# Kernel optimization log

Hardware: AMD Instinct MI355X
Metric: run time of the kernel (lower is better)

Reference implementation:

```python
import jax, jax.numpy as jnp
import numpy as np

D = 1024
H = 16
HD = D // H

def setup_inputs() -> dict:
    key = jax.random.key(0)
    ks = jax.random.split(key, 6)
    tokens = jax.random.normal(ks[0], (2, 2048, D), dtype=jnp.float32)
    # LayerNorm params
    ln_gamma = jnp.ones((D,), dtype=jnp.float32)
    ln_beta = jnp.zeros((D,), dtype=jnp.float32)
    # qkv Linear (no bias): torch Linear weight is [3D, D]; store as [D, 3D] for x @ W
    w_qkv = jax.random.normal(ks[1], (D, 3 * D), dtype=jnp.float32) / np.sqrt(D)
    # output projection with bias
    w_proj = jax.random.normal(ks[2], (D, D), dtype=jnp.float32) / np.sqrt(D)
    b_proj = jax.random.normal(ks[3], (D,), dtype=jnp.float32) * 0.01
    return {"tokens": tokens, "ln_gamma": ln_gamma, "ln_beta": ln_beta,
            "w_qkv": w_qkv, "w_proj": w_proj, "b_proj": b_proj}

def reference(tokens, ln_gamma, ln_beta, w_qkv, w_proj, b_proj):
    B, S, _ = tokens.shape
    res = tokens
    # LayerNorm (eps=1e-5, torch default)
    mu = jnp.mean(tokens, axis=-1, keepdims=True)
    var = jnp.var(tokens, axis=-1, keepdims=True)
    x = (tokens - mu) * jax.lax.rsqrt(var + 1e-5) * ln_gamma + ln_beta
    # QKV projection -> [B, S, 3, H, HD] -> q,k,v each [B, H, S, HD]
    qkv = (x @ w_qkv).reshape(B, S, 3, H, HD)
    qkv = jnp.transpose(qkv, (2, 0, 3, 1, 4))
    q, k, v = qkv[0], qkv[1], qkv[2]
    scale = HD ** -0.5
    scores = jnp.einsum('bhsd,bhtd->bhst', q, k) * scale  # [B,H,S,S]
    attn = jax.nn.softmax(scores, axis=-1)
    dots = jnp.einsum('bhst,bhtd->bhsd', attn, v)          # [B,H,S,HD]
    dots = jnp.transpose(dots, (0, 2, 1, 3)).reshape(B, S, D)
    out = dots @ w_proj + b_proj
    return out + res
```

## Files before the change

### kernel.cpp

```cpp
#include <hip/hip_runtime.h>

typedef __bf16 bf16x8 __attribute__((ext_vector_type(8)));
typedef __bf16 bf16x4 __attribute__((ext_vector_type(4)));
typedef float f32x4 __attribute__((ext_vector_type(4)));
typedef unsigned short us8 __attribute__((ext_vector_type(8)));

__device__ __forceinline__ unsigned short f2bf(float f) {
  unsigned int u = __builtin_bit_cast(unsigned int, f);
  u += 0x7FFFu + ((u >> 16) & 1u);
  return (unsigned short)(u >> 16);
}
__device__ __forceinline__ float bf2f(unsigned short s) {
  return __builtin_bit_cast(float, (unsigned int)s << 16);
}

__device__ __forceinline__ void load_lds16(const void* g, void* l) {
  __builtin_amdgcn_global_load_lds(
      (const __attribute__((address_space(1))) unsigned int*)g,
      (__attribute__((address_space(3))) unsigned int*)l, 16, 0, 0);
}

#define MFMA16(a, b, c) __builtin_amdgcn_mfma_f32_16x16x32_bf16(a, b, c, 0, 0, 0)
#define EXP2(x) __builtin_amdgcn_exp2f(x)

constexpr int Dm = 1024, Ss = 2048;

__global__ __launch_bounds__(256) void prep_kernel(
    const float* __restrict__ x, const float* __restrict__ gamma,
    const float* __restrict__ beta, unsigned short* __restrict__ xbf,
    const float* __restrict__ wqkv, unsigned short* __restrict__ wqkvT,
    const float* __restrict__ wproj, unsigned short* __restrict__ wprojT) {
  __shared__ float tile[32][33];
  const int t = threadIdx.x;
  if (blockIdx.x < 4096) {
    const int row = blockIdx.x;
    const float4 v = reinterpret_cast<const float4*>(x + (size_t)row * Dm)[t];
    float s = v.x + v.y + v.z + v.w;
    float ss = v.x * v.x + v.y * v.y + v.z * v.z + v.w * v.w;
#pragma unroll
    for (int off = 1; off < 64; off <<= 1) {
      s += __shfl_xor(s, off);
      ss += __shfl_xor(ss, off);
    }
    float* sb = &tile[0][0];
    const int lane = t & 63, wid = t >> 6;
    if (lane == 0) { sb[wid] = s; sb[4 + wid] = ss; }
    __syncthreads();
    s = sb[0] + sb[1] + sb[2] + sb[3];
    ss = sb[4] + sb[5] + sb[6] + sb[7];
    const float mu = s * (1.0f / Dm);
    const float var = ss * (1.0f / Dm) - mu * mu;
    const float rs = rsqrtf(var + 1e-5f);
    const float4 g = reinterpret_cast<const float4*>(gamma)[t];
    const float4 bt = reinterpret_cast<const float4*>(beta)[t];
    ushort4 pack;
    pack.x = f2bf((v.x - mu) * rs * g.x + bt.x);
    pack.y = f2bf((v.y - mu) * rs * g.y + bt.y);
    pack.z = f2bf((v.z - mu) * rs * g.z + bt.z);
    pack.w = f2bf((v.w - mu) * rs * g.w + bt.w);
    reinterpret_cast<ushort4*>(xbf + (size_t)row * Dm)[t] = pack;
  } else {
    const float* in;
    unsigned short* out;
    int N, bxi, byi;
    const int id0 = blockIdx.x - 4096;
    if (id0 < 3072) {
      in = wqkv; out = wqkvT; N = 3072;
      bxi = id0 % 96; byi = id0 / 96;
    } else {
      in = wproj; out = wprojT; N = 1024;
      const int id = id0 - 3072;
      bxi = id % 32; byi = id / 32;
    }
    const int tx = t & 31, ty = t >> 5;
    const int n0 = bxi * 32, k0 = byi * 32;
#pragma unroll
    for (int i = 0; i < 4; i++)
      tile[ty + i * 8][tx] = in[(size_t)(k0 + ty + i * 8) * N + n0 + tx];
    __syncthreads();
#pragma unroll
    for (int i = 0; i < 4; i++)
      out[(size_t)(n0 + ty + i * 8) * 1024 + k0 + tx] = f2bf(tile[tx][ty + i * 8]);
  }
}

__global__ __launch_bounds__(512) void gemm256_kernel(
    const unsigned short* __restrict__ A, const unsigned short* __restrict__ Bt,
    unsigned short* __restrict__ Cbf, unsigned short* __restrict__ vt) {
  extern __shared__ char lds[];
  const int tid = threadIdx.x;
  const int lane = tid & 63, wid = tid >> 6;
  const int l15 = lane & 15, lg = lane >> 4;
  const int wr = wid >> 2, wc = wid & 3;
  const int lb = (blockIdx.x & 7) * 24 + (blockIdx.x >> 3);
  const int bx = lb % 12, by = lb / 12;
  const int bm = by * 256, bn = bx * 256;
  const int sswz = ((lane & 3) * 16) ^ (((lane >> 3) & 3) << 4);
  const char* Asrc = (const char*)A + (size_t)(bm + wid * 32 + (lane >> 2)) * 2048 + sswz;
  const char* Bsrc = (const char*)Bt + (size_t)(bn + wid * 32 + (lane >> 2)) * 2048 + sswz;
  const int rdsz = ((lg * 16) ^ (((l15 >> 1) & 3) << 4));

#define STG_A(kk_, bufT, tile_)                                                 \
  if ((tile_) < 16) {                                                           \
    _Pragma("unroll") for (int c = 0; c < 2; c++)                               \
      load_lds16(Asrc + (size_t)(c * 16) * 2048 + (tile_) * 128 + (kk_) * 64,   \
                 lds + ((bufT) * 2 + (kk_)) * 16384 + wid * 2048 + c * 1024);   \
  }
#define STG_B(kk_, bufT, tile_)                                                 \
  if ((tile_) < 16) {                                                           \
    _Pragma("unroll") for (int c = 0; c < 2; c++)                               \
      load_lds16(Bsrc + (size_t)(c * 16) * 2048 + (tile_) * 128 + (kk_) * 64,   \
                 lds + 65536 + ((bufT) * 2 + (kk_)) * 16384 + wid * 2048 +      \
                     c * 1024);                                                 \
  }
#define DS_A(buf_, kk_)                                                         \
  _Pragma("unroll") for (int mi = 0; mi < 8; mi++) {                            \
    const int r = wr * 128 + mi * 16 + l15;                                     \
    af[mi] = *(const bf16x8*)(lds + ((buf_) * 2 + (kk_)) * 16384 + r * 64 + rdsz); \
  }
#define DS_B(buf_, kk_, nh_)                                                    \
  _Pragma("unroll") for (int nj = 0; nj < 2; nj++) {                            \
    const int r = wc * 64 + (nh_) * 32 + nj * 16 + l15;                         \
    bfr[nj] = *(const bf16x8*)(lds + 65536 + ((buf_) * 2 + (kk_)) * 16384 +     \
                               r * 64 + rdsz);                                  \
  }
#define MM(nh_)                                                                 \
  __builtin_amdgcn_s_setprio(1);                                                \
  _Pragma("unroll") for (int mi = 0; mi < 8; mi++)                              \
      _Pragma("unroll") for (int nj = 0; nj < 2; nj++)                          \
          acc[mi][(nh_) * 2 + nj] = MFMA16(af[mi], bfr[nj], acc[mi][(nh_) * 2 + nj]); \
  __builtin_amdgcn_s_setprio(0);
#define GBAR __builtin_amdgcn_s_barrier()
#define LGKM0 asm volatile("s_waitcnt lgkmcnt(0)" ::: "memory")

  f32x4 acc[8][4] = {};

  STG_A(0, 0, 0); STG_B(0, 0, 0); STG_A(1, 0, 0); STG_B(1, 0, 0);
  STG_A(0, 1, 1); STG_B(0, 1, 1); STG_A(1, 1, 1);
  asm volatile("s_waitcnt vmcnt(6)" ::: "memory");
  GBAR;

  for (int i = 0; i < 8; ++i) {
    const int t2 = 2 * i + 2, t3 = 2 * i + 3;
    const bool last = (i == 7);
    bf16x8 af[8], bfr[2];
    DS_A(0, 0); DS_B(0, 0, 0); STG_B(1, 1, 2 * i + 1);
    GBAR; LGKM0; MM(0); GBAR;
    DS_B(0, 0, 1); STG_A(0, 0, t2);
    GBAR; LGKM0; MM(1); GBAR;
    DS_A(0, 1); DS_B(0, 1, 0); STG_B(0, 0, t2);
    GBAR; LGKM0; MM(0); GBAR;
    DS_B(0, 1, 1); STG_A(1, 0, t2);
    GBAR; LGKM0; MM(1);
    if (last) asm volatile("s_waitcnt vmcnt(0)" ::: "memory");
    else      asm volatile("s_waitcnt vmcnt(6)" ::: "memory");
    GBAR;
    DS_A(1, 0); DS_B(1, 0, 0); STG_B(1, 0, t2);
    GBAR; LGKM0; MM(0); GBAR;
    DS_B(1, 0, 1); STG_A(0, 1, t3);
    GBAR; LGKM0; MM(1); GBAR;
    DS_A(1, 1); DS_B(1, 1, 0); STG_B(0, 1, t3);
    GBAR; LGKM0; MM(0); GBAR;
    DS_B(1, 1, 1); STG_A(1, 1, t3);
    GBAR; LGKM0; MM(1);
    if (last) asm volatile("s_waitcnt vmcnt(0)" ::: "memory");
    else      asm volatile("s_waitcnt vmcnt(6)" ::: "memory");
    GBAR;
  }

#pragma unroll
  for (int mi = 0; mi < 8; mi++)
#pragma unroll
    for (int nj = 0; nj < 4; nj++) {
      const int m = bm + wr * 128 + mi * 16 + lg * 4;
      const int n = bn + wc * 64 + nj * 16 + l15;
      if (n < 2048) {
        const float sc = (n < 1024) ? 0.180336880f : 1.0f;
#pragma unroll
        for (int r = 0; r < 4; r++)
          Cbf[(size_t)(m + r) * 3072 + n] = f2bf(acc[mi][nj][r] * sc);
      } else {
        const int h = (n - 2048) >> 6, hd = (n - 2048) & 63;
        const int bq = m >> 11, s = m & 2047;
        bf16x4 o;
#pragma unroll
        for (int r = 0; r < 4; r++) o[r] = (__bf16)acc[mi][nj][r];
        *(bf16x4*)(vt + ((size_t)((bq << 4) + h) * 64 + hd) * 2048 + s) = o;
      }
    }
#undef STG_A
#undef STG_B
#undef DS_A
#undef DS_B
#undef MM
#undef GBAR
#undef LGKM0
}

__global__ __launch_bounds__(256) void gemm_proj_kernel(
    const unsigned short* __restrict__ A, const unsigned short* __restrict__ Bt,
    float* __restrict__ Cf, const float* __restrict__ bias,
    const float* __restrict__ resid) {
  __shared__ unsigned short Al[2][128 * 64];
  __shared__ unsigned short Bl[2][64 * 64];
  const int tid = threadIdx.x;
  const int lane = tid & 63, wid = tid >> 6;
  const int l15 = lane & 15, lg = lane >> 4;
  const int wm = wid >> 1, wn = wid & 1;
  const int cpx = gridDim.x >> 3;
  const int lb = (blockIdx.x & 7) * cpx + (blockIdx.x >> 3);
  const int bx = lb % 16, by = lb / 16;
  const int bm = by * 128, bn = bx * 64;
  const int r8 = lane >> 3;
  const int swz = ((lane & 7) * 16) ^ (r8 << 4);
  const char* Ab = (const char*)A;
  const char* Bb = (const char*)Bt;
  f32x4 acc[4][2] = {};

#define PSTAGE(bufi, k0v)                                                      \
  {                                                                            \
    _Pragma("unroll") for (int p = 0; p < 4; p++) {                            \
      const int row = p * 32 + wid * 8 + r8;                                   \
      load_lds16(Ab + ((size_t)(bm + row) * 1024 + (k0v)) * 2 + swz,           \
                 (char*)&Al[bufi][0] + p * 4096 + wid * 1024);                 \
    }                                                                          \
    _Pragma("unroll") for (int p = 0; p < 2; p++) {                            \
      const int row = p * 32 + wid * 8 + r8;                                   \
      load_lds16(Bb + ((size_t)(bn + row) * 1024 + (k0v)) * 2 + swz,           \
                 (char*)&Bl[bufi][0] + p * 4096 + wid * 1024);                 \
    }                                                                          \
  }

  PSTAGE(0, 0);

  for (int it = 0; it < 16; it++) {
    const int cur = it & 1;
    asm volatile("s_waitcnt vmcnt(0)" ::: "memory");
    __builtin_amdgcn_s_barrier();
    if (it + 1 < 16) PSTAGE(cur ^ 1, (it + 1) * 64);

#pragma unroll
    for (int kk = 0; kk < 2; kk++) {
      bf16x8 af[4], bfr[2];
#pragma unroll
      for (int mi = 0; mi < 4; mi++) {
        const int row = wm * 64 + mi * 16 + l15;
        af[mi] = *(const bf16x8*)((const char*)&Al[cur][0] + row * 128 +
                                  ((kk * 64 + lg * 16) ^ ((row & 7) << 4)));
      }
#pragma unroll
      for (int nj = 0; nj < 2; nj++) {
        const int row = wn * 32 + nj * 16 + l15;
        bfr[nj] = *(const bf16x8*)((const char*)&Bl[cur][0] + row * 128 +
                                   ((kk * 64 + lg * 16) ^ ((row & 7) << 4)));
      }
      __builtin_amdgcn_s_setprio(1);
#pragma unroll
      for (int mi = 0; mi < 4; mi++)
#pragma unroll
        for (int nj = 0; nj < 2; nj++)
          acc[mi][nj] = MFMA16(af[mi], bfr[nj], acc[mi][nj]);
      __builtin_amdgcn_s_setprio(0);
    }
  }

#pragma unroll
  for (int mi = 0; mi < 4; mi++)
#pragma unroll
    for (int nj = 0; nj < 2; nj++) {
      const int m = bm + wm * 64 + mi * 16 + lg * 4;
      const int n = bn + wn * 32 + nj * 16 + l15;
#pragma unroll
      for (int r = 0; r < 4; r++) {
        const size_t idx = (size_t)(m + r) * 1024 + n;
        Cf[idx] = acc[mi][nj][r] + bias[n] + resid[idx];
      }
    }
#undef PSTAGE
}

__global__ __launch_bounds__(512) void attn_kernel(
    const unsigned short* __restrict__ qkv, const unsigned short* __restrict__ vt,
    unsigned short* part0, unsigned short* part1, float* __restrict__ ml) {
  __shared__ unsigned short Kb[2][64 * 64];
  __shared__ unsigned short Vb[2][64 * 64];
  __shared__ unsigned short Pl[8][32][64];
  const int tid = threadIdx.x, lane = tid & 63, wid = tid >> 6;
  const int l15 = lane & 15, lg = lane >> 4;
  const int lb = (blockIdx.x & 7) * 64 + (blockIdx.x >> 3);
  const int bh = lb >> 4, qt = (lb >> 1) & 7, half = lb & 1;
  const int b = bh >> 4, h = bh & 15;
  const int q0 = qt * 256 + wid * 32;
  const unsigned short* qbase = qkv + (size_t)(b * Ss) * 3072 + h * 64;
  const char* kbase = (const char*)(qkv + (size_t)(b * Ss) * 3072 + 1024 + h * 64);
  const char* vbase = (const char*)(vt + (size_t)bh * 64 * Ss);

  bf16x8 qf[2][2];
#pragma unroll
  for (int qj = 0; qj < 2; qj++)
#pragma unroll
    for (int kk = 0; kk < 2; kk++)
      qf[qj][kk] = *reinterpret_cast<const bf16x8*>(
          &qbase[(size_t)(q0 + qj * 16 + l15) * 3072 + kk * 32 + lg * 8]);

  f32x4 accT[4][2] = {};
  float psum[2] = {0.f, 0.f};

  const int srow = lane >> 3;
  const int swz = ((lane & 7) * 16) ^ (srow << 4);

#define STAGE(bufi, t0v)                                                          \
  {                                                                               \
    load_lds16(kbase + (size_t)((t0v) + wid * 8 + srow) * 6144 + swz,             \
               (char*)&Kb[bufi][0] + wid * 1024);                                 \
    load_lds16(vbase + (size_t)(wid * 8 + srow) * 4096 + (size_t)(t0v) * 2 + swz, \
               (char*)&Vb[bufi][0] + wid * 1024);                                 \
  }

  const int t0base = half * 1024;
  STAGE(0, t0base);

  for (int itr = 0; itr < 16; itr++) {
    const int cur = itr & 1;
    asm volatile("s_waitcnt vmcnt(0)" ::: "memory");
    __builtin_amdgcn_s_barrier();
    if (itr + 1 < 16) STAGE(cur ^ 1, t0base + (itr + 1) * 64);

    const char* kcur = (const char*)&Kb[cur][0];
    const char* vcur = (const char*)&Vb[cur][0];

    f32x4 accs[4][2] = {};
    __builtin_amdgcn_s_setprio(1);
#pragma unroll
    for (int kk = 0; kk < 2; kk++) {
      bf16x8 kf[4];
#pragma unroll
      for (int kvi = 0; kvi < 4; kvi++) {
        const int rk = kvi * 16 + l15;
        kf[kvi] = *(const bf16x8*)(kcur + rk * 128 +
                                   ((kk * 64 + lg * 16) ^ ((rk & 7) << 4)));
      }
#pragma unroll
      for (int kvi = 0; kvi < 4; kvi++)
#pragma unroll
        for (int qj = 0; qj < 2; qj++)
          accs[kvi][qj] = MFMA16(kf[kvi], qf[qj][kk], accs[kvi][qj]);
    }
    __builtin_amdgcn_s_setprio(0);

#pragma unroll
    for (int qj = 0; qj < 2; qj++) {
      const int prow = qj * 16 + l15;
      char* prl = (char*)&Pl[wid][prow][0];
      float ps = 0.f;
#pragma unroll
      for (int kvi = 0; kvi < 4; kvi++) {
        bf16x4 pk;
#pragma unroll
        for (int r = 0; r < 4; r++) {
          const float p = EXP2(accs[kvi][qj][r]);
          ps += p;
          pk[r] = (__bf16)p;
        }
        *(bf16x4*)(prl + ((kvi * 32 + lg * 8) ^ ((l15 & 7) << 4))) = pk;
      }
      psum[qj] += ps;
    }

    asm volatile("s_waitcnt lgkmcnt(0)" ::: "memory");
    __builtin_amdgcn_sched_barrier(0);

    __builtin_amdgcn_s_setprio(1);
#pragma unroll
    for (int kk2 = 0; kk2 < 2; kk2++) {
      bf16x8 pf[2], vf[4];
#pragma unroll
      for (int qj = 0; qj < 2; qj++)
        pf[qj] = *(const bf16x8*)((const char*)&Pl[wid][qj * 16 + l15][0] +
                                  ((kk2 * 64 + lg * 16) ^ ((l15 & 7) << 4)));
#pragma unroll
      for (int nj = 0; nj < 4; nj++) {
        const int rv = nj * 16 + l15;
        vf[nj] = *(const bf16x8*)(vcur + rv * 128 +
                                  ((kk2 * 64 + lg * 16) ^ ((rv & 7) << 4)));
      }
#pragma unroll
      for (int nj = 0; nj < 4; nj++)
#pragma unroll
        for (int qj = 0; qj < 2; qj++)
          accT[nj][qj] = MFMA16(vf[nj], pf[qj], accT[nj][qj]);
    }
    __builtin_amdgcn_s_setprio(0);
  }

#pragma unroll
  for (int qj = 0; qj < 2; qj++) {
    psum[qj] += __shfl_xor(psum[qj], 16);
    psum[qj] += __shfl_xor(psum[qj], 32);
  }
  unsigned short* pout = half ? part1 : part0;
#pragma unroll
  for (int qj = 0; qj < 2; qj++) {
    const float rl = 1.0f / psum[qj];
    const int q = q0 + qj * 16 + l15;
#pragma unroll
    for (int nj = 0; nj < 4; nj++) {
      bf16x4 o;
#pragma unroll
      for (int r = 0; r < 4; r++) o[r] = (__bf16)(accT[nj][qj][r] * rl);
      *(bf16x4*)(pout + (size_t)(b * Ss + q) * Dm + h * 64 + nj * 16 + lg * 4) = o;
    }
  }
  if (lg == 0) {
#pragma unroll
    for (int qj = 0; qj < 2; qj++)
      ml[half * 65536 + bh * 2048 + q0 + qj * 16 + l15] = psum[qj];
  }
}

__global__ __launch_bounds__(256) void combine_kernel(
    const unsigned short* p0, const unsigned short* __restrict__ p1,
    const float* __restrict__ ml, unsigned short* dots) {
  const int t = blockIdx.x * 256 + threadIdx.x;
  const int hd8 = t & 7;
  const int h = (t >> 3) & 15;
  const int row = t >> 7;
  const int b = row >> 11, s = row & 2047;
  const int bh = b * 16 + h;
  const float w0 = ml[bh * 2048 + s];
  const float w1 = ml[65536 + bh * 2048 + s];
  const float inv = 1.0f / (w0 + w1);
  const size_t off = (size_t)row * 1024 + h * 64 + hd8 * 8;
  const us8 a = *(const us8*)(p0 + off);
  const us8 c = *(const us8*)(p1 + off);
  us8 o;
#pragma unroll
  for (int j = 0; j < 8; j++)
    o[j] = f2bf((bf2f(a[j]) * w0 + bf2f(c[j]) * w1) * inv);
  *(us8*)(dots + off) = o;
}

extern "C" void kernel_launch(void* const* d_in, const int* in_sizes, int n_in,
                              void* d_out, int out_size, void* d_ws, size_t ws_size,
                              hipStream_t stream) {
  const float* tokens = (const float*)d_in[0];
  const float* ln_g = (const float*)d_in[1];
  const float* ln_b = (const float*)d_in[2];
  const float* w_qkv = (const float*)d_in[3];
  const float* w_proj = (const float*)d_in[4];
  const float* b_proj = (const float*)d_in[5];
  float* out = (float*)d_out;

  char* ws = (char*)d_ws;
  unsigned short* x_bf = (unsigned short*)(ws);
  unsigned short* wqkvT = (unsigned short*)(ws + 8388608);
  unsigned short* wprojT = (unsigned short*)(ws + 14680064);
  unsigned short* qkvraw = (unsigned short*)(ws + 16777216);
  unsigned short* vt = (unsigned short*)(ws + 41943040);
  unsigned short* part1 = (unsigned short*)(ws + 50331648);
  float* ml = (float*)(ws + 58720256);
  unsigned short* dots = x_bf;

  hipFuncSetAttribute((const void*)gemm256_kernel,
                      hipFuncAttributeMaxDynamicSharedMemorySize, 131072);

  prep_kernel<<<8192, 256, 0, stream>>>(tokens, ln_g, ln_b, x_bf,
                                        w_qkv, wqkvT, w_proj, wprojT);
  gemm256_kernel<<<192, 512, 131072, stream>>>(x_bf, wqkvT, qkvraw, vt);
  attn_kernel<<<512, 512, 0, stream>>>(qkvraw, vt, dots, part1, ml);
  combine_kernel<<<2048, 256, 0, stream>>>(dots, part1, ml, dots);
  gemm_proj_kernel<<<512, 256, 0, stream>>>(dots, wprojT, out, b_proj, tokens);
}
```

Baseline: 113.0 us.

## Fuse split-KV attention combine into projection GEMM A-tile loading

Removes the separate combine kernel and instead merges the two partial attention outputs, weighted by their softmax sums, while staging the A operand of the output-projection GEMM. A tiles are now loaded through registers, combined and written to LDS by the threads, rather than sent asynchronously by global_load_lds. This drops one launch and the write and re-read of the combined dots buffer. In exchange each projection block reads two partial tensors, and the 16 N-blocks sharing each M-tile now redo the combine, adding VALU work and register pressure to the GEMM main loop.

```diff
diff --git a/kernel.cpp b/kernel.cpp
--- a/kernel.cpp
+++ b/kernel.cpp
@@ -198,7 +198,8 @@
 }
 
 __global__ __launch_bounds__(256) void gemm_proj_kernel(
-    const unsigned short* __restrict__ A, const unsigned short* __restrict__ Bt,
+    const unsigned short* __restrict__ p0, const unsigned short* __restrict__ p1,
+    const float* __restrict__ ml, const unsigned short* __restrict__ Bt,
     float* __restrict__ Cf, const float* __restrict__ bias,
     const float* __restrict__ resid) {
   __shared__ unsigned short Al[2][128 * 64];
@@ -213,16 +214,22 @@
   const int bm = by * 128, bn = bx * 64;
   const int r8 = lane >> 3;
   const int swz = ((lane & 7) * 16) ^ (r8 << 4);
-  const char* Ab = (const char*)A;
   const char* Bb = (const char*)Bt;
   f32x4 acc[4][2] = {};
 
-#define PSTAGE(bufi, k0v)                                                      \
+  us8 pa[4], pc[4];
+  float w0r[4], w1r[4];
+
+#define PLOAD(bufi, k0v, itv)                                                  \
   {                                                                            \
     _Pragma("unroll") for (int p = 0; p < 4; p++) {                            \
-      const int row = p * 32 + wid * 8 + r8;                                   \
-      load_lds16(Ab + ((size_t)(bm + row) * 1024 + (k0v)) * 2 + swz,           \
-                 (char*)&Al[bufi][0] + p * 4096 + wid * 1024);                 \
+      const int row = bm + p * 32 + wid * 8 + r8;                              \
+      const size_t ab = (size_t)row * 2048 + (size_t)(k0v) * 2 + swz;          \
+      pa[p] = *(const us8*)((const char*)p0 + ab);                             \
+      pc[p] = *(const us8*)((const char*)p1 + ab);                             \
+      const int bq = row >> 11, s = row & 2047;                                \
+      w0r[p] = ml[(bq * 16 + (itv)) * 2048 + s];                               \
+      w1r[p] = ml[65536 + (bq * 16 + (itv)) * 2048 + s];                       \
     }                                                                          \
     _Pragma("unroll") for (int p = 0; p < 2; p++) {                            \
       const int row = p * 32 + wid * 8 + r8;                                   \
@@ -231,13 +238,24 @@
     }                                                                          \
   }
 
-  PSTAGE(0, 0);
+  PLOAD(0, 0, 0);
 
   for (int it = 0; it < 16; it++) {
     const int cur = it & 1;
     asm volatile("s_waitcnt vmcnt(0)" ::: "memory");
+#pragma unroll
+    for (int p = 0; p < 4; p++) {
+      const float inv = 1.0f / (w0r[p] + w1r[p]);
+      const float w0 = w0r[p] * inv, w1 = w1r[p] * inv;
+      us8 o;
+#pragma unroll
+      for (int j = 0; j < 8; j++)
+        o[j] = f2bf(bf2f(pa[p][j]) * w0 + bf2f(pc[p][j]) * w1);
+      *(us8*)((char*)&Al[cur][0] + p * 4096 + wid * 1024 + lane * 16) = o;
+    }
+    asm volatile("s_waitcnt lgkmcnt(0)" ::: "memory");
     __builtin_amdgcn_s_barrier();
-    if (it + 1 < 16) PSTAGE(cur ^ 1, (it + 1) * 64);
+    if (it + 1 < 16) PLOAD(cur ^ 1, (it + 1) * 64, it + 1);
 
 #pragma unroll
     for (int kk = 0; kk < 2; kk++) {
@@ -276,7 +294,7 @@
         Cf[idx] = acc[mi][nj][r] + bias[n] + resid[idx];
       }
     }
-#undef PSTAGE
+#undef PLOAD
 }
 
 __global__ __launch_bounds__(512) void attn_kernel(
@@ -418,28 +436,6 @@
   }
 }
 
-__global__ __launch_bounds__(256) void combine_kernel(
-    const unsigned short* p0, const unsigned short* __restrict__ p1,
-    const float* __restrict__ ml, unsigned short* dots) {
-  const int t = blockIdx.x * 256 + threadIdx.x;
-  const int hd8 = t & 7;
-  const int h = (t >> 3) & 15;
-  const int row = t >> 7;
-  const int b = row >> 11, s = row & 2047;
-  const int bh = b * 16 + h;
-  const float w0 = ml[bh * 2048 + s];
-  const float w1 = ml[65536 + bh * 2048 + s];
-  const float inv = 1.0f / (w0 + w1);
-  const size_t off = (size_t)row * 1024 + h * 64 + hd8 * 8;
-  const us8 a = *(const us8*)(p0 + off);
-  const us8 c = *(const us8*)(p1 + off);
-  us8 o;
-#pragma unroll
-  for (int j = 0; j < 8; j++)
-    o[j] = f2bf((bf2f(a[j]) * w0 + bf2f(c[j]) * w1) * inv);
-  *(us8*)(dots + off) = o;
-}
-
 extern "C" void kernel_launch(void* const* d_in, const int* in_sizes, int n_in,
                               void* d_out, int out_size, void* d_ws, size_t ws_size,
                               hipStream_t stream) {
@@ -459,7 +455,7 @@
   unsigned short* vt = (unsigned short*)(ws + 41943040);
   unsigned short* part1 = (unsigned short*)(ws + 50331648);
   float* ml = (float*)(ws + 58720256);
-  unsigned short* dots = x_bf;
+  unsigned short* part0 = x_bf;
 
   hipFuncSetAttribute((const void*)gemm256_kernel,
                       hipFuncAttributeMaxDynamicSharedMemorySize, 131072);
@@ -467,7 +463,7 @@
   prep_kernel<<<8192, 256, 0, stream>>>(tokens, ln_g, ln_b, x_bf,
                                         w_qkv, wqkvT, w_proj, wprojT);
   gemm256_kernel<<<192, 512, 131072, stream>>>(x_bf, wqkvT, qkvraw, vt);
-  attn_kernel<<<512, 512, 0, stream>>>(qkvraw, vt, dots, part1, ml);
-  combine_kernel<<<2048, 256, 0, stream>>>(dots, part1, ml, dots);
-  gemm_proj_kernel<<<512, 256, 0, stream>>>(dots, wprojT, out, b_proj, tokens);
-}
+  attn_kernel<<<512, 512, 0, stream>>>(qkvraw, vt, part0, part1, ml);
+  gemm_proj_kernel<<<512, 256, 0, stream>>>(part0, part1, ml, wprojT, out,
+                                            b_proj, tokens);
+}
```

New measurement: 121.1 us. +7.2%, slower.
